# Performance work log

Measured on AMD Instinct MI355X. Metric: run time of the kernel, lower is better.

Reference implementation:

```python
import math
import jax, jax.numpy as jnp
from jax import lax
import numpy as np

NUM_EXPERTS = 8
TOP_K = 2
CAPACITY_FACTOR = 1.25
AUX_COEF = 0.01


def setup_inputs() -> dict:
    key = jax.random.key(0)
    k1, k2, k3, k4, k5 = jax.random.split(key, 5)
    B, T, C, I, E = 4, 2048, 768, 3072, NUM_EXPERTS
    x = jax.random.normal(k1, (B, T, C), dtype=jnp.float32)
    Wr = jax.random.normal(k2, (C, E), dtype=jnp.float32) * 0.02
    Wg = jax.random.normal(k3, (E, C, I), dtype=jnp.float32) * 0.02
    Wu = jax.random.normal(k4, (E, C, I), dtype=jnp.float32) * 0.02
    Wp = jax.random.normal(k5, (E, I, C), dtype=jnp.float32) * 0.02
    return {"x": x, "Wr": Wr, "Wg": Wg, "Wu": Wu, "Wp": Wp}


def reference(x, Wr, Wg, Wu, Wp):
    E, K = NUM_EXPERTS, TOP_K
    B, T, C = x.shape
    N = B * T
    capacity = max(1, math.ceil(CAPACITY_FACTOR * N / E))  # static: 1280
    xf = x.reshape(N, C)

    # --- router ---
    logits = xf @ Wr                                    # [N, E]
    probs = jax.nn.softmax(logits.astype(jnp.float32), axis=-1)
    gates, idx = lax.top_k(probs, K)                    # [N, 2] each
    gates = gates / jnp.clip(jnp.sum(gates, axis=-1, keepdims=True), 1e-9)

    # --- aux load-balancing loss ---
    oh1 = jax.nn.one_hot(idx[:, 0], E, dtype=jnp.int32)  # [N, E]
    oh2 = jax.nn.one_hot(idx[:, 1], E, dtype=jnp.int32)
    importance = probs.mean(axis=0)
    load = (oh1 + oh2).astype(jnp.float32).mean(axis=0) / K
    aux_loss = jnp.sum(importance * load) * E * AUX_COEF

    # --- capacity positions (running rank within each expert) ---
    pos1 = jnp.sum((jnp.cumsum(oh1, axis=0) - 1) * oh1, axis=-1)   # [N]
    mask1 = pos1 < capacity
    slot1 = idx[:, 0] * capacity + pos1
    count1 = jnp.minimum(jnp.sum(oh1, axis=0), capacity)           # [E]
    pos2 = jnp.sum((jnp.cumsum(oh2, axis=0) - 1) * oh2, axis=-1) + count1[idx[:, 1]]
    mask2 = pos2 < capacity
    slot2 = idx[:, 1] * capacity + pos2

    # --- dispatch (scatter into per-expert buffers; OOB slots dropped) ---
    buf = jnp.zeros((E * capacity, C), dtype=x.dtype)
    s1 = jnp.where(mask1, slot1, E * capacity)
    s2 = jnp.where(mask2, slot2, E * capacity)
    buf = buf.at[s1].set(xf, mode='drop')
    buf = buf.at[s2].set(xf, mode='drop')
    ein = buf.reshape(E, capacity, C)

    # --- per-expert swiglu MLP (grouped GEMMs) ---
    gate = jax.nn.silu(jnp.einsum('enc,ech->enh', ein, Wg))
    up = jnp.einsum('enc,ech->enh', ein, Wu)
    out = jnp.einsum('enh,ehc->enc', gate * up, Wp).reshape(E * capacity, C)

    # --- combine (gather back to token order, renormalized gates) ---
    g1 = gates[:, 0] * mask1.astype(jnp.float32)
    g2 = gates[:, 1] * mask2.astype(jnp.float32)
    denom = jnp.clip(g1 + g2, 1e-9)
    g1 = (g1 / denom).astype(x.dtype)
    g2 = (g2 / denom).astype(x.dtype)
    c1 = jnp.clip(slot1, 0, E * capacity - 1)
    c2 = jnp.clip(slot2, 0, E * capacity - 1)
    y = g1[:, None] * out[c1] + g2[:, None] * out[c2]
    return y.reshape(B, T, C), aux_loss
```

## Files before the change

kernel.cpp:

```cpp
#include <hip/hip_runtime.h>
#include <cstdint>
#include <cstddef>

#define NTOK 8192
#define NEXP 8
#define CAP 1280
#define CDIM 768
#define IDIM 3072
#define EROWS (NEXP*CAP)

typedef __attribute__((ext_vector_type(8))) short short8;
typedef __attribute__((ext_vector_type(4))) float f32x4;
typedef __attribute__((ext_vector_type(4))) unsigned short us4;
typedef __attribute__((ext_vector_type(8))) unsigned short us8;

__device__ __forceinline__ unsigned short f2b(float f) {
  unsigned u = __builtin_bit_cast(unsigned, f);
  u += 0x7FFFu + ((u >> 16) & 1u);
  return (unsigned short)(u >> 16);
}

__global__ __launch_bounds__(256) void transpose_cvt64(const float* __restrict__ src,
    unsigned short* __restrict__ dst, int R, int S) {
  int tilesS = S >> 6, tilesR = R >> 6;
  int perE = tilesR * tilesS;
  int e = blockIdx.x / perE;
  int rem = blockIdx.x % perE;
  int rt = rem / tilesS, st = rem % tilesS;
  const float* se = src + (size_t)e*R*S + ((size_t)rt*64)*S + st*64;
  unsigned short* de = dst + (size_t)e*R*S + ((size_t)st*64)*R + rt*64;
  __shared__ float tile[64][65];
  int c4 = (threadIdx.x & 15)*4, rr = threadIdx.x >> 4;
#pragma unroll
  for (int p = 0; p < 4; ++p) {
    float4 v = *(const float4*)(se + (size_t)(rr + 16*p)*S + c4);
    tile[rr + 16*p][c4+0] = v.x; tile[rr + 16*p][c4+1] = v.y;
    tile[rr + 16*p][c4+2] = v.z; tile[rr + 16*p][c4+3] = v.w;
  }
  __syncthreads();
#pragma unroll
  for (int p = 0; p < 4; ++p) {
    int s = rr + 16*p;
    us4 o;
    o.x = f2b(tile[c4+0][s]); o.y = f2b(tile[c4+1][s]);
    o.z = f2b(tile[c4+2][s]); o.w = f2b(tile[c4+3][s]);
    *(us4*)(de + (size_t)s*R + c4) = o;
  }
}

__global__ __launch_bounds__(256) void wgu_cvt64(const float* __restrict__ Wg,
    const float* __restrict__ Wu, unsigned short* __restrict__ Wgu) {
  const int tilesR = CDIM/64, tilesS = IDIM/64;
  const int perE = tilesR * tilesS;
  int sel = blockIdx.x / (NEXP*perE);
  int rem = blockIdx.x % (NEXP*perE);
  int e = rem / perE; int r2 = rem % perE;
  int rt = r2 / tilesS, st = r2 % tilesS;
  const float* se = (sel ? Wu : Wg) + (size_t)e*CDIM*IDIM + ((size_t)rt*64)*IDIM + st*64;
  __shared__ float tile[64][65];
  int c4 = (threadIdx.x & 15)*4, rr = threadIdx.x >> 4;
#pragma unroll
  for (int p = 0; p < 4; ++p) {
    float4 v = *(const float4*)(se + (size_t)(rr + 16*p)*IDIM + c4);
    tile[rr + 16*p][c4+0] = v.x; tile[rr + 16*p][c4+1] = v.y;
    tile[rr + 16*p][c4+2] = v.z; tile[rr + 16*p][c4+3] = v.w;
  }
  __syncthreads();
  unsigned short* dstE = Wgu + (size_t)e*(2*IDIM)*CDIM;
#pragma unroll
  for (int p = 0; p < 4; ++p) {
    int s = rr + 16*p;
    int np = 128*st + 32*(s>>4) + (s&15) + sel*16;
    us4 o;
    o.x = f2b(tile[c4+0][s]); o.y = f2b(tile[c4+1][s]);
    o.z = f2b(tile[c4+2][s]); o.w = f2b(tile[c4+3][s]);
    *(us4*)(dstE + (size_t)np*CDIM + rt*64 + c4) = o;
  }
}

__global__ __launch_bounds__(256) void router_kernel(const float* __restrict__ x,
    const float* __restrict__ Wr, float* __restrict__ probs,
    int* __restrict__ idx1, int* __restrict__ idx2,
    float* __restrict__ g1r, float* __restrict__ g2r) {
  __shared__ float WrT[NEXP*CDIM];
  for (int i = threadIdx.x; i < NEXP*CDIM; i += 256) {
    int c = i >> 3, e = i & 7;
    WrT[e*CDIM + c] = Wr[i];
  }
  __syncthreads();
  int w = threadIdx.x >> 6, l = threadIdx.x & 63;
  int t = blockIdx.x*4 + w;
  float acc[NEXP];
#pragma unroll
  for (int e = 0; e < NEXP; ++e) acc[e] = 0.f;
  for (int k = 0; k < CDIM/64; ++k) {
    float xv = x[(size_t)t*CDIM + k*64 + l];
#pragma unroll
    for (int e = 0; e < NEXP; ++e) acc[e] += xv * WrT[e*CDIM + k*64 + l];
  }
#pragma unroll
  for (int off = 32; off > 0; off >>= 1) {
#pragma unroll
    for (int e = 0; e < NEXP; ++e) acc[e] += __shfl_xor(acc[e], off);
  }
  if (l == 0) {
    float m = acc[0];
#pragma unroll
    for (int e = 1; e < NEXP; ++e) m = fmaxf(m, acc[e]);
    float p[NEXP]; float s = 0.f;
#pragma unroll
    for (int e = 0; e < NEXP; ++e) { p[e] = expf(acc[e] - m); s += p[e]; }
    float inv = 1.f / s;
#pragma unroll
    for (int e = 0; e < NEXP; ++e) { p[e] *= inv; probs[(size_t)t*NEXP + e] = p[e]; }
    int i1 = 0; float b1 = p[0];
#pragma unroll
    for (int e = 1; e < NEXP; ++e) if (p[e] > b1) { b1 = p[e]; i1 = e; }
    int i2 = -1; float b2 = -1e30f;
#pragma unroll
    for (int e = 0; e < NEXP; ++e) if (e != i1 && p[e] > b2) { b2 = p[e]; i2 = e; }
    float gs = fmaxf(b1 + b2, 1e-9f);
    g1r[t] = b1 / gs; g2r[t] = b2 / gs;
    idx1[t] = i1; idx2[t] = i2;
  }
}

__global__ __launch_bounds__(1024) void scan_kernel(
    const int* __restrict__ idx1, const int* __restrict__ idx2,
    const float* __restrict__ g1r, const float* __restrict__ g2r,
    const float* __restrict__ probs,
    int* __restrict__ bufmap,
    int* __restrict__ c1o, int* __restrict__ c2o,
    float* __restrict__ g1o, float* __restrict__ g2o,
    float* __restrict__ aux_out) {
  __shared__ unsigned int scanbuf[1024][9];
  __shared__ unsigned int totals[NEXP];
  int tid = threadIdx.x;
  int e1[8], e2[8];
  unsigned int cnt[NEXP];
#pragma unroll
  for (int k = 0; k < NEXP; ++k) cnt[k] = 0;
  for (int j = 0; j < 8; ++j) {
    int t = tid*8 + j;
    e1[j] = idx1[t]; e2[j] = idx2[t];
    cnt[e1[j]] += 1u;
    cnt[e2[j]] += (1u << 16);
  }
#pragma unroll
  for (int k = 0; k < NEXP; ++k) scanbuf[tid][k] = cnt[k];
  unsigned int run[NEXP];
#pragma unroll
  for (int k = 0; k < NEXP; ++k) run[k] = cnt[k];
  __syncthreads();
  for (int off = 1; off < 1024; off <<= 1) {
    unsigned int add[NEXP];
#pragma unroll
    for (int k = 0; k < NEXP; ++k) add[k] = 0;
    if (tid >= off) {
#pragma unroll
      for (int k = 0; k < NEXP; ++k) add[k] = scanbuf[tid - off][k];
    }
    __syncthreads();
#pragma unroll
    for (int k = 0; k < NEXP; ++k) { run[k] += add[k]; scanbuf[tid][k] = run[k]; }
    __syncthreads();
  }
  if (tid == 1023) {
#pragma unroll
    for (int k = 0; k < NEXP; ++k) totals[k] = run[k];
  }
  __syncthreads();
  unsigned int excl[NEXP];
#pragma unroll
  for (int k = 0; k < NEXP; ++k) excl[k] = run[k] - cnt[k];
  int cnt1c[NEXP];
#pragma unroll
  for (int k = 0; k < NEXP; ++k) cnt1c[k] = min((int)(totals[k] & 0xFFFFu), CAP);

  for (int j = 0; j < 8; ++j) {
    int t = tid*8 + j;
    int a = e1[j];
    int pos1 = (int)(excl[a] & 0xFFFFu); excl[a] += 1u;
    int slot1 = a*CAP + pos1;
    bool m1 = pos1 < CAP;
    if (m1) bufmap[slot1] = t;
    int b = e2[j];
    int pos2 = (int)(excl[b] >> 16) + cnt1c[b]; excl[b] += (1u << 16);
    int slot2 = b*CAP + pos2;
    bool m2 = pos2 < CAP;
    if (m2) bufmap[slot2] = t;
    float G1 = m1 ? g1r[t] : 0.f;
    float G2 = m2 ? g2r[t] : 0.f;
    float den = fmaxf(G1 + G2, 1e-9f);
    g1o[t] = G1 / den; g2o[t] = G2 / den;
    c1o[t] = min(slot1, EROWS - 1);
    c2o[t] = min(slot2, EROWS - 1);
  }

  float imp[NEXP];
#pragma unroll
  for (int k = 0; k < NEXP; ++k) imp[k] = 0.f;
  for (int j = 0; j < 8; ++j) {
    int t = tid*8 + j;
    const float4* pr = (const float4*)(probs + (size_t)t*NEXP);
    float4 a0 = pr[0], a1 = pr[1];
    imp[0] += a0.x; imp[1] += a0.y; imp[2] += a0.z; imp[3] += a0.w;
    imp[4] += a1.x; imp[5] += a1.y; imp[6] += a1.z; imp[7] += a1.w;
  }
  __syncthreads();
  float* fbuf = (float*)&scanbuf[0][0];
#pragma unroll
  for (int k = 0; k < NEXP; ++k) fbuf[tid*9 + k] = imp[k];
  __syncthreads();
  for (int s = 512; s >= 1; s >>= 1) {
    if (tid < s) {
#pragma unroll
      for (int k = 0; k < NEXP; ++k) fbuf[tid*9 + k] += fbuf[(tid + s)*9 + k];
    }
    __syncthreads();
  }
  if (tid == 0) {
    float aux = 0.f;
#pragma unroll
    for (int k = 0; k < NEXP; ++k) {
      float importance = fbuf[k] / (float)NTOK;
      float loadk = (float)((totals[k] & 0xFFFFu) + (totals[k] >> 16)) / ((float)NTOK * 2.0f);
      aux += importance * loadk;
    }
    aux_out[0] = aux * (float)NEXP * 0.01f;
  }
}

__global__ __launch_bounds__(192) void dispatch_kernel(const float* __restrict__ x,
    const int* __restrict__ bufmap, unsigned short* __restrict__ ein) {
  int r = blockIdx.x;
  int t = bufmap[r];
  int q = threadIdx.x;
  float4 v = make_float4(0.f, 0.f, 0.f, 0.f);
  if (t >= 0) v = ((const float4*)x)[(size_t)t*(CDIM/4) + q];
  us4 o;
  o.x = f2b(v.x); o.y = f2b(v.y); o.z = f2b(v.z); o.w = f2b(v.w);
  ((us4*)ein)[(size_t)r*(CDIM/4) + q] = o;
}

#define BAR  asm volatile("s_barrier" ::: "memory")
#define VMW(N) asm volatile("s_waitcnt vmcnt(" #N ")" ::: "memory")
#define P1 __builtin_amdgcn_s_setprio(1)
#define P0 __builtin_amdgcn_s_setprio(0)

template<int KD>
__global__ __launch_bounds__(512, 2) void gemm1_8ph(
    const unsigned short* __restrict__ A,
    const unsigned short* __restrict__ Bw,
    unsigned short* __restrict__ H) {
  constexpr int NT = KD/64;
  constexpr int NITER = NT/2;
  __shared__ unsigned short lds[65536];

  const int bid = blockIdx.x;
  const int chunk = gridDim.x >> 3;
  const int tile = (bid & 7)*chunk + (bid >> 3);
  const int e = tile / 120;
  const int rem = tile % 120;
  const int nt = rem / 5, mt = rem % 5;

  const int tid = threadIdx.x;
  const int l = tid & 63, wid = tid >> 6;
  const int wr = wid >> 2, wc = wid & 3;
  const int lrow = l & 15, khi = l >> 4;

  const unsigned short* Ab = A  + (size_t)e*CAP*KD    + (size_t)mt*256*KD;
  const unsigned short* Bb = Bw + (size_t)e*(2*IDIM)*KD + (size_t)nt*256*KD;

  const int srow = tid >> 3;
  const int scol = (tid & 7) ^ (srow & 7);
  const size_t lane_off = (size_t)srow*KD + scol*8;
  const int lds_st = wid*512;

#define STG(buf, op, half, kt) do { \
    const unsigned short* s_ = ((op) ? Bb : Ab) + lane_off + (size_t)(half)*128*KD + (size_t)(kt)*64; \
    unsigned short* d_ = (unsigned short*)lds + (buf)*32768 + (op)*16384 + (half)*8192 + lds_st; \
    __builtin_amdgcn_global_load_lds((const __attribute__((address_space(1))) void*)s_, \
        (__attribute__((address_space(3))) void*)d_, 16, 0, 0); \
    __builtin_amdgcn_global_load_lds((const __attribute__((address_space(1))) void*)(s_ + (size_t)64*KD), \
        (__attribute__((address_space(3))) void*)(d_ + 4096), 16, 0, 0); \
  } while(0)

  const int swz0 = ((khi    ) ^ (lrow & 7)) * 8;
  const int swz1 = ((4 + khi) ^ (lrow & 7)) * 8;
  const int abase = wr*8192 + lrow*64;
  const int bbase = 16384 + (wc>>1)*8192 + ((wc&1)*64 + lrow)*64;

#define LDA(buf, dst, mb) do { _Pragma("unroll") for (int m_=0;m_<4;++m_) { \
    dst[m_][0] = *(const short8*)(lds + (buf)*32768 + abase + ((mb)+m_)*1024 + swz0); \
    dst[m_][1] = *(const short8*)(lds + (buf)*32768 + abase + ((mb)+m_)*1024 + swz1); } } while(0)
#define LDB(buf, dst, nb) do { _Pragma("unroll") for (int n_=0;n_<2;++n_) { \
    dst[n_][0] = *(const short8*)(lds + (buf)*32768 + bbase + ((nb)+n_)*1024 + swz0); \
    dst[n_][1] = *(const short8*)(lds + (buf)*32768 + bbase + ((nb)+n_)*1024 + swz1); } } while(0)
#define QUAD(af, bf, mb, nb) do { _Pragma("unroll") for (int r_=0;r_<2;++r_) \
    _Pragma("unroll") for (int n_=0;n_<2;++n_) \
    _Pragma("unroll") for (int m_=0;m_<4;++m_) \
      acc[(mb)+m_][(nb)+n_] = __builtin_amdgcn_mfma_f32_16x16x32_bf16(af[m_][r_], bf[n_][r_], acc[(mb)+m_][(nb)+n_], 0,0,0); } while(0)

  f32x4 acc[8][4];
#pragma unroll
  for (int i = 0; i < 8; ++i)
#pragma unroll
    for (int j = 0; j < 4; ++j) acc[i][j] = (f32x4){0.f,0.f,0.f,0.f};

  short8 a[4][2], bl[2][2], bh[2][2];

  STG(0,0,0,0); STG(0,0,1,0); STG(0,1,0,0); STG(0,1,1,0);
  STG(1,1,0,1); STG(1,1,1,1); STG(1,0,0,1);
  VMW(6);
  BAR;

#define ITER(tY, t2, t3, DOS2, VM4, VM8) \
    LDA(0,a,0); LDB(0,bl,0); STG(1,0,1,(tY)); \
    BAR; P1; QUAD(a,bl,0,0); P0; BAR; \
    LDB(0,bh,2); \
    BAR; P1; QUAD(a,bh,0,2); P0; BAR; \
    LDA(0,a,4); if (DOS2) STG(0,1,0,(t2)); \
    BAR; P1; QUAD(a,bh,4,2); P0; BAR; \
    if (DOS2) STG(0,1,1,(t2)); VM4; \
    BAR; P1; QUAD(a,bl,4,0); P0; BAR; \
    LDA(1,a,0); LDB(1,bl,0); if (DOS2) STG(0,0,0,(t2)); \
    BAR; P1; QUAD(a,bl,0,0); P0; BAR; \
    LDB(1,bh,2); if (DOS2) STG(0,0,1,(t2)); \
    BAR; P1; QUAD(a,bh,0,2); P0; BAR; \
    LDA(1,a,4); if (DOS2) STG(1,1,0,(t3)); \
    BAR; P1; QUAD(a,bh,4,2); P0; BAR; \
    if (DOS2) { STG(1,1,1,(t3)); STG(1,0,0,(t3)); } VM8; \
    BAR; P1; QUAD(a,bl,4,0); P0; BAR;

#pragma unroll 1
  for (int i = 0; i < NITER-1; ++i) {
    const int tY = 2*i+1, t2 = 2*i+2, t3 = 2*i+3;
    ITER(tY, t2, t3, true, VMW(4), VMW(6));
  }
  ITER(NT-1, 0, 0, false, VMW(0), VMW(0));

#undef ITER
#undef QUAD
#undef LDB
#undef LDA
#undef STG

  __syncthreads();
  {
    const int cb0 = wc*32 + lrow;
    const int rb0 = wr*128 + khi*4;
#pragma unroll
    for (int m = 0; m < 8; ++m)
#pragma unroll
      for (int p = 0; p < 2; ++p) {
        f32x4 g = acc[m][2*p], u = acc[m][2*p+1];
#pragma unroll
        for (int r = 0; r < 4; ++r) {
          float gv = g[r];
          float hv = gv / (1.f + __expf(-gv)) * u[r];
          lds[(rb0 + m*16 + r)*136 + cb0 + p*16] = f2b(hv);
        }
      }
  }
  __syncthreads();
  const size_t rowg = (size_t)e*CAP + (size_t)mt*256;
  const size_t colg = (size_t)nt*128 + (size_t)(l & 15)*8;
#pragma unroll
  for (int i = 0; i < 8; ++i) {
    int row = wid*32 + i*4 + (l >> 4);
    us8 v = *(const us8*)(lds + row*136 + (l & 15)*8);
    *(us8*)(H + (rowg + row)*(size_t)IDIM + colg) = v;
  }
}

template<int K, bool NOUTER>
__global__ __launch_bounds__(256, 2) void gemm_bt(
    const unsigned short* __restrict__ A,
    const unsigned short* __restrict__ B0,
    float* __restrict__ Fout,
    int Ntiles, int N) {
  constexpr int MT = 10;
  int chunk = gridDim.x >> 3;
  int bid = blockIdx.x;
  int tile = (bid & 7)*chunk + (bid >> 3);
  int perE = MT * Ntiles;
  int e = tile / perE, rem = tile % perE;
  int mt, nt;
  if (NOUTER) { nt = rem / MT; mt = rem % MT; }
  else        { mt = rem / Ntiles; nt = rem % Ntiles; }

  const unsigned short* Ae  = A  + (size_t)e*CAP*K + (size_t)mt*128*K;
  const unsigned short* B0e = B0 + (size_t)e*N*K   + (size_t)nt*128*K;

  __shared__ unsigned short Alds[128*64];
  __shared__ unsigned short B0lds[128*64];

  int tid = threadIdx.x;
  int l = tid & 63, w = tid >> 6;
  int rbase = w*8 + (l >> 3);
  int csrc  = (l & 7) ^ ((l >> 3) & 7);
  size_t gbase = (size_t)rbase*K + (size_t)csrc*8;
  int ldsoff = w*512;

  f32x4 acc0[16];
#pragma unroll
  for (int i = 0; i < 16; ++i) acc0[i] = (f32x4){0.f,0.f,0.f,0.f};

  int wm = (w >> 1)*64, wn = (w & 1)*64;
  int lrow = l & 15, khi = l >> 4;

  for (int kt = 0; kt < K/64; ++kt) {
    const unsigned short* Ag  = Ae  + gbase + (size_t)kt*64;
    const unsigned short* Bg0 = B0e + gbase + (size_t)kt*64;
#pragma unroll
    for (int q = 0; q < 4; ++q) {
      __builtin_amdgcn_global_load_lds(
          (const __attribute__((address_space(1))) void*)(Ag + (size_t)q*32*K),
          (__attribute__((address_space(3))) void*)(Alds + ldsoff + q*2048), 16, 0, 0);
    }
#pragma unroll
    for (int q = 0; q < 4; ++q) {
      __builtin_amdgcn_global_load_lds(
          (const __attribute__((address_space(1))) void*)(Bg0 + (size_t)q*32*K),
          (__attribute__((address_space(3))) void*)(B0lds + ldsoff + q*2048), 16, 0, 0);
    }
    __syncthreads();
#pragma unroll
    for (int kk = 0; kk < 2; ++kk) {
      int cs = (kk*4 + khi) ^ (l & 7);
      short8 af[4];
#pragma unroll
      for (int m = 0; m < 4; ++m) {
        int row = wm + m*16 + lrow;
        af[m] = *(const short8*)(Alds + row*64 + cs*8);
      }
#pragma unroll
      for (int n = 0; n < 4; ++n) {
        int rowb = wn + n*16 + lrow;
        short8 b0 = *(const short8*)(B0lds + rowb*64 + cs*8);
#pragma unroll
        for (int m = 0; m < 4; ++m)
          acc0[m*4+n] = __builtin_amdgcn_mfma_f32_16x16x32_bf16(af[m], b0, acc0[m*4+n], 0, 0, 0);
      }
    }
    __syncthreads();
  }

  float* Fp = Fout + (size_t)e*CAP*N + (size_t)mt*128*N + (size_t)nt*128;
#pragma unroll
  for (int m = 0; m < 4; ++m) {
#pragma unroll
    for (int n = 0; n < 4; ++n) {
      f32x4 v = acc0[m*4+n];
#pragma unroll
      for (int r = 0; r < 4; ++r) {
        int row = wm + m*16 + khi*4 + r;
        int col = wn + n*16 + lrow;
        Fp[(size_t)row*N + col] = v[r];
      }
    }
  }
}

__global__ __launch_bounds__(192) void combine_kernel(const float* __restrict__ outbuf,
    const int* __restrict__ c1, const int* __restrict__ c2,
    const float* __restrict__ g1, const float* __restrict__ g2,
    float* __restrict__ y) {
  int t = blockIdx.x;
  int q = threadIdx.x;
  float f1 = g1[t], f2 = g2[t];
  int a = c1[t], b = c2[t];
  float4 va = ((const float4*)outbuf)[(size_t)a*(CDIM/4) + q];
  float4 vb = ((const float4*)outbuf)[(size_t)b*(CDIM/4) + q];
  float4 r;
  r.x = f1*va.x + f2*vb.x;
  r.y = f1*va.y + f2*vb.y;
  r.z = f1*va.z + f2*vb.z;
  r.w = f1*va.w + f2*vb.w;
  ((float4*)y)[(size_t)t*(CDIM/4) + q] = r;
}

extern "C" void kernel_launch(void* const* d_in, const int* in_sizes, int n_in,
                              void* d_out, int out_size, void* d_ws, size_t ws_size,
                              hipStream_t stream) {
  const float* x  = (const float*)d_in[0];
  const float* Wr = (const float*)d_in[1];
  const float* Wg = (const float*)d_in[2];
  const float* Wu = (const float*)d_in[3];
  const float* Wp = (const float*)d_in[4];
  float* y = (float*)d_out;

  char* p = (char*)d_ws;
  auto alloc = [&](size_t bytes) { char* r = p; p += (bytes + 255) & ~(size_t)255; return r; };
  unsigned short* WguT = (unsigned short*)alloc((size_t)NEXP*2*IDIM*CDIM*2);
  unsigned short* WpT  = (unsigned short*)alloc((size_t)NEXP*CDIM*IDIM*2);
  unsigned short* ein  = (unsigned short*)alloc((size_t)EROWS*CDIM*2);
  unsigned short* h    = (unsigned short*)alloc((size_t)EROWS*IDIM*2);
  float* outbuf = (float*)alloc((size_t)EROWS*CDIM*4);
  float* probs  = (float*)alloc((size_t)NTOK*NEXP*4);
  int* idx1 = (int*)alloc(NTOK*4);
  int* idx2 = (int*)alloc(NTOK*4);
  int* c1   = (int*)alloc(NTOK*4);
  int* c2   = (int*)alloc(NTOK*4);
  float* g1r = (float*)alloc(NTOK*4);
  float* g2r = (float*)alloc(NTOK*4);
  float* g1o = (float*)alloc(NTOK*4);
  float* g2o = (float*)alloc(NTOK*4);
  int* bufmap = (int*)alloc(EROWS*4);

  size_t required = (size_t)(p - (char*)d_ws);
  if (ws_size < required) return;

  hipMemsetAsync(bufmap, 0xFF, EROWS*sizeof(int), stream);

  wgu_cvt64<<<2*NEXP*(CDIM/64)*(IDIM/64), 256, 0, stream>>>(Wg, Wu, WguT);
  transpose_cvt64<<<NEXP*(IDIM/64)*(CDIM/64), 256, 0, stream>>>(Wp, WpT, IDIM, CDIM);

  router_kernel<<<NTOK/4, 256, 0, stream>>>(x, Wr, probs, idx1, idx2, g1r, g2r);
  scan_kernel<<<1, 1024, 0, stream>>>(idx1, idx2, g1r, g2r, probs, bufmap,
                                      c1, c2, g1o, g2o, y + (size_t)NTOK*CDIM);
  dispatch_kernel<<<EROWS, 192, 0, stream>>>(x, bufmap, ein);

  gemm1_8ph<CDIM><<<NEXP*5*(2*IDIM/256), 512, 0, stream>>>(ein, WguT, h);
  gemm_bt<IDIM, false><<<NEXP*10*(CDIM/128), 256, 0, stream>>>(
      h, WpT, outbuf, CDIM/128, CDIM);

  combine_kernel<<<NTOK, 192, 0, stream>>>(outbuf, c1, c2, g1o, g2o, y);
}
```

Measured before the change: 316.8 us.

## Triple-buffer B operand in gate/up GEMM and store down-proj output as bf16

The gate/up GEMM grows LDS from 128KB to 160KB so the weight operand gets three rotating buffers while A stays double-buffered. This lets weight tiles be prefetched further ahead and hides global load latency better. Separately, the down-projection GEMM now writes bf16 through an LDS-staged, coalesced store instead of scattered fp32 writes, and the combine kernel reads bf16. This halves output traffic but drops output precision to bf16 and may lower occupancy of the first GEMM.

```diff
diff --git a/kernel.cpp b/kernel.cpp
--- a/kernel.cpp
+++ b/kernel.cpp
@@ -18,6 +18,9 @@
   unsigned u = __builtin_bit_cast(unsigned, f);
   u += 0x7FFFu + ((u >> 16) & 1u);
   return (unsigned short)(u >> 16);
+}
+__device__ __forceinline__ float b2f(unsigned short u) {
+  return __builtin_bit_cast(float, ((unsigned)u) << 16);
 }
 
 __global__ __launch_bounds__(256) void transpose_cvt64(const float* __restrict__ src,
@@ -255,7 +258,7 @@
     unsigned short* __restrict__ H) {
   constexpr int NT = KD/64;
   constexpr int NITER = NT/2;
-  __shared__ unsigned short lds[65536];
+  __shared__ unsigned short lds[81920];
 
   const int bid = blockIdx.x;
   const int chunk = gridDim.x >> 3;
@@ -269,7 +272,7 @@
   const int wr = wid >> 2, wc = wid & 3;
   const int lrow = l & 15, khi = l >> 4;
 
-  const unsigned short* Ab = A  + (size_t)e*CAP*KD    + (size_t)mt*256*KD;
+  const unsigned short* Ab = A  + (size_t)e*CAP*KD      + (size_t)mt*256*KD;
   const unsigned short* Bb = Bw + (size_t)e*(2*IDIM)*KD + (size_t)nt*256*KD;
 
   const int srow = tid >> 3;
@@ -277,9 +280,9 @@
   const size_t lane_off = (size_t)srow*KD + scol*8;
   const int lds_st = wid*512;
 
-#define STG(buf, op, half, kt) do { \
-    const unsigned short* s_ = ((op) ? Bb : Ab) + lane_off + (size_t)(half)*128*KD + (size_t)(kt)*64; \
-    unsigned short* d_ = (unsigned short*)lds + (buf)*32768 + (op)*16384 + (half)*8192 + lds_st; \
+#define STG(dstu, srcp, half, kt) do { \
+    const unsigned short* s_ = (srcp) + lane_off + (size_t)(half)*128*KD + (size_t)(kt)*64; \
+    unsigned short* d_ = (unsigned short*)lds + (dstu) + (half)*8192 + lds_st; \
     __builtin_amdgcn_global_load_lds((const __attribute__((address_space(1))) void*)s_, \
         (__attribute__((address_space(3))) void*)d_, 16, 0, 0); \
     __builtin_amdgcn_global_load_lds((const __attribute__((address_space(1))) void*)(s_ + (size_t)64*KD), \
@@ -288,15 +291,15 @@
 
   const int swz0 = ((khi    ) ^ (lrow & 7)) * 8;
   const int swz1 = ((4 + khi) ^ (lrow & 7)) * 8;
-  const int abase = wr*8192 + lrow*64;
-  const int bbase = 16384 + (wc>>1)*8192 + ((wc&1)*64 + lrow)*64;
-
-#define LDA(buf, dst, mb) do { _Pragma("unroll") for (int m_=0;m_<4;++m_) { \
-    dst[m_][0] = *(const short8*)(lds + (buf)*32768 + abase + ((mb)+m_)*1024 + swz0); \
-    dst[m_][1] = *(const short8*)(lds + (buf)*32768 + abase + ((mb)+m_)*1024 + swz1); } } while(0)
-#define LDB(buf, dst, nb) do { _Pragma("unroll") for (int n_=0;n_<2;++n_) { \
-    dst[n_][0] = *(const short8*)(lds + (buf)*32768 + bbase + ((nb)+n_)*1024 + swz0); \
-    dst[n_][1] = *(const short8*)(lds + (buf)*32768 + bbase + ((nb)+n_)*1024 + swz1); } } while(0)
+  const int aoff = wr*8192 + lrow*64;
+  const int boff = (wc>>1)*8192 + ((wc&1)*64 + lrow)*64;
+
+#define LDA(ab, dst, mb) do { _Pragma("unroll") for (int m_=0;m_<4;++m_) { \
+    dst[m_][0] = *(const short8*)(lds + (ab) + aoff + ((mb)+m_)*1024 + swz0); \
+    dst[m_][1] = *(const short8*)(lds + (ab) + aoff + ((mb)+m_)*1024 + swz1); } } while(0)
+#define LDB(bb, dst, nb) do { _Pragma("unroll") for (int n_=0;n_<2;++n_) { \
+    dst[n_][0] = *(const short8*)(lds + (bb) + boff + ((nb)+n_)*1024 + swz0); \
+    dst[n_][1] = *(const short8*)(lds + (bb) + boff + ((nb)+n_)*1024 + swz1); } } while(0)
 #define QUAD(af, bf, mb, nb) do { _Pragma("unroll") for (int r_=0;r_<2;++r_) \
     _Pragma("unroll") for (int n_=0;n_<2;++n_) \
     _Pragma("unroll") for (int m_=0;m_<4;++m_) \
@@ -310,35 +313,40 @@
 
   short8 a[4][2], bl[2][2], bh[2][2];
 
-  STG(0,0,0,0); STG(0,0,1,0); STG(0,1,0,0); STG(0,1,1,0);
-  STG(1,1,0,1); STG(1,1,1,1); STG(1,0,0,1);
-  VMW(6);
+  int bA_ = 32768, bB_ = 49152, bC_ = 65536;
+
+  STG(0, Ab, 0, 0);      STG(bA_, Bb, 0, 0);
+  STG(0, Ab, 1, 0);      STG(bA_, Bb, 1, 0);
+  STG(16384, Ab, 0, 1);  STG(bB_, Bb, 0, 1);
+  STG(16384, Ab, 1, 1);  STG(bB_, Bb, 1, 1);
+  VMW(8);
   BAR;
 
-#define ITER(tY, t2, t3, DOS2, VM4, VM8) \
-    LDA(0,a,0); LDB(0,bl,0); STG(1,0,1,(tY)); \
-    BAR; P1; QUAD(a,bl,0,0); P0; BAR; \
-    LDB(0,bh,2); \
-    BAR; P1; QUAD(a,bh,0,2); P0; BAR; \
-    LDA(0,a,4); if (DOS2) STG(0,1,0,(t2)); \
-    BAR; P1; QUAD(a,bh,4,2); P0; BAR; \
-    if (DOS2) STG(0,1,1,(t2)); VM4; \
-    BAR; P1; QUAD(a,bl,4,0); P0; BAR; \
-    LDA(1,a,0); LDB(1,bl,0); if (DOS2) STG(0,0,0,(t2)); \
-    BAR; P1; QUAD(a,bl,0,0); P0; BAR; \
-    LDB(1,bh,2); if (DOS2) STG(0,0,1,(t2)); \
-    BAR; P1; QUAD(a,bh,0,2); P0; BAR; \
-    LDA(1,a,4); if (DOS2) STG(1,1,0,(t3)); \
-    BAR; P1; QUAD(a,bh,4,2); P0; BAR; \
-    if (DOS2) { STG(1,1,1,(t3)); STG(1,0,0,(t3)); } VM8; \
-    BAR; P1; QUAD(a,bl,4,0); P0; BAR;
+#define ITER(t2, t3, DOS, VM4, VM8) \
+    LDA(0, a, 0); LDB(bA_, bl, 0); if (DOS) STG(bC_, Bb, 0, (t2)); \
+    BAR; P1; QUAD(a, bl, 0, 0); P0; BAR; \
+    LDB(bA_, bh, 2); if (DOS) STG(bC_, Bb, 1, (t2)); \
+    BAR; P1; QUAD(a, bh, 0, 2); P0; BAR; \
+    LDA(0, a, 4); \
+    BAR; P1; QUAD(a, bh, 4, 2); P0; BAR; \
+    if (DOS) STG(0, Ab, 0, (t2)); VM4; \
+    BAR; P1; QUAD(a, bl, 4, 0); P0; BAR; \
+    LDA(16384, a, 0); LDB(bB_, bl, 0); if (DOS) { STG(0, Ab, 1, (t2)); STG(bA_, Bb, 0, (t3)); } \
+    BAR; P1; QUAD(a, bl, 0, 0); P0; BAR; \
+    LDB(bB_, bh, 2); if (DOS) STG(bA_, Bb, 1, (t3)); \
+    BAR; P1; QUAD(a, bh, 0, 2); P0; BAR; \
+    LDA(16384, a, 4); \
+    BAR; P1; QUAD(a, bh, 4, 2); P0; BAR; \
+    if (DOS) { STG(16384, Ab, 0, (t3)); STG(16384, Ab, 1, (t3)); } VM8; \
+    BAR; P1; QUAD(a, bl, 4, 0); P0; BAR;
 
 #pragma unroll 1
   for (int i = 0; i < NITER-1; ++i) {
-    const int tY = 2*i+1, t2 = 2*i+2, t3 = 2*i+3;
-    ITER(tY, t2, t3, true, VMW(4), VMW(6));
-  }
-  ITER(NT-1, 0, 0, false, VMW(0), VMW(0));
+    const int t2 = 2*i+2, t3 = 2*i+3;
+    ITER(t2, t3, true, VMW(6), VMW(8));
+    int tmp = bC_; bC_ = bB_; bB_ = bA_; bA_ = tmp;
+  }
+  ITER(0, 0, false, VMW(0), VMW(0));
 
 #undef ITER
 #undef QUAD
@@ -374,11 +382,11 @@
   }
 }
 
-template<int K, bool NOUTER>
+template<int K>
 __global__ __launch_bounds__(256, 2) void gemm_bt(
     const unsigned short* __restrict__ A,
     const unsigned short* __restrict__ B0,
-    float* __restrict__ Fout,
+    unsigned short* __restrict__ Fout,
     int Ntiles, int N) {
   constexpr int MT = 10;
   int chunk = gridDim.x >> 3;
@@ -386,15 +394,14 @@
   int tile = (bid & 7)*chunk + (bid >> 3);
   int perE = MT * Ntiles;
   int e = tile / perE, rem = tile % perE;
-  int mt, nt;
-  if (NOUTER) { nt = rem / MT; mt = rem % MT; }
-  else        { mt = rem / Ntiles; nt = rem % Ntiles; }
+  int mt = rem / Ntiles, nt = rem % Ntiles;
 
   const unsigned short* Ae  = A  + (size_t)e*CAP*K + (size_t)mt*128*K;
   const unsigned short* B0e = B0 + (size_t)e*N*K   + (size_t)nt*128*K;
 
-  __shared__ unsigned short Alds[128*64];
-  __shared__ unsigned short B0lds[128*64];
+  __shared__ unsigned short sh[16384];
+  unsigned short* Alds = sh;
+  unsigned short* B0lds = sh + 8192;
 
   int tid = threadIdx.x;
   int l = tid & 63, w = tid >> 6;
@@ -447,23 +454,34 @@
     __syncthreads();
   }
 
-  float* Fp = Fout + (size_t)e*CAP*N + (size_t)mt*128*N + (size_t)nt*128;
-#pragma unroll
-  for (int m = 0; m < 4; ++m) {
-#pragma unroll
-    for (int n = 0; n < 4; ++n) {
-      f32x4 v = acc0[m*4+n];
-#pragma unroll
-      for (int r = 0; r < 4; ++r) {
-        int row = wm + m*16 + khi*4 + r;
-        int col = wn + n*16 + lrow;
-        Fp[(size_t)row*N + col] = v[r];
-      }
-    }
-  }
-}
-
-__global__ __launch_bounds__(192) void combine_kernel(const float* __restrict__ outbuf,
+  const size_t rowg = (size_t)e*CAP + (size_t)mt*128;
+  const size_t colg = (size_t)nt*128;
+#pragma unroll
+  for (int h = 0; h < 2; ++h) {
+    if ((w >> 1) == h) {
+#pragma unroll
+      for (int m = 0; m < 4; ++m)
+#pragma unroll
+        for (int n = 0; n < 4; ++n) {
+          f32x4 v = acc0[m*4+n];
+#pragma unroll
+          for (int r = 0; r < 4; ++r)
+            sh[(m*16 + khi*4 + r)*136 + wn + n*16 + lrow] = f2b(v[r]);
+        }
+    }
+    __syncthreads();
+#pragma unroll
+    for (int jj = 0; jj < 4; ++jj) {
+      int idx = tid + 256*jj;
+      int rp = idx >> 4, ch = idx & 15;
+      us8 v = *(const us8*)(sh + rp*136 + ch*8);
+      *(us8*)(Fout + (rowg + h*64 + rp)*(size_t)N + colg + ch*8) = v;
+    }
+    __syncthreads();
+  }
+}
+
+__global__ __launch_bounds__(192) void combine_kernel(const unsigned short* __restrict__ outbuf,
     const int* __restrict__ c1, const int* __restrict__ c2,
     const float* __restrict__ g1, const float* __restrict__ g2,
     float* __restrict__ y) {
@@ -471,13 +489,13 @@
   int q = threadIdx.x;
   float f1 = g1[t], f2 = g2[t];
   int a = c1[t], b = c2[t];
-  float4 va = ((const float4*)outbuf)[(size_t)a*(CDIM/4) + q];
-  float4 vb = ((const float4*)outbuf)[(size_t)b*(CDIM/4) + q];
+  us4 va = ((const us4*)outbuf)[(size_t)a*(CDIM/4) + q];
+  us4 vb = ((const us4*)outbuf)[(size_t)b*(CDIM/4) + q];
   float4 r;
-  r.x = f1*va.x + f2*vb.x;
-  r.y = f1*va.y + f2*vb.y;
-  r.z = f1*va.z + f2*vb.z;
-  r.w = f1*va.w + f2*vb.w;
+  r.x = f1*b2f(va.x) + f2*b2f(vb.x);
+  r.y = f1*b2f(va.y) + f2*b2f(vb.y);
+  r.z = f1*b2f(va.z) + f2*b2f(vb.z);
+  r.w = f1*b2f(va.w) + f2*b2f(vb.w);
   ((float4*)y)[(size_t)t*(CDIM/4) + q] = r;
 }
 
@@ -497,7 +515,7 @@
   unsigned short* WpT  = (unsigned short*)alloc((size_t)NEXP*CDIM*IDIM*2);
   unsigned short* ein  = (unsigned short*)alloc((size_t)EROWS*CDIM*2);
   unsigned short* h    = (unsigned short*)alloc((size_t)EROWS*IDIM*2);
-  float* outbuf = (float*)alloc((size_t)EROWS*CDIM*4);
+  unsigned short* outbuf = (unsigned short*)alloc((size_t)EROWS*CDIM*2);
   float* probs  = (float*)alloc((size_t)NTOK*NEXP*4);
   int* idx1 = (int*)alloc(NTOK*4);
   int* idx2 = (int*)alloc(NTOK*4);
@@ -523,7 +541,7 @@
   dispatch_kernel<<<EROWS, 192, 0, stream>>>(x, bufmap, ein);
 
   gemm1_8ph<CDIM><<<NEXP*5*(2*IDIM/256), 512, 0, stream>>>(ein, WguT, h);
-  gemm_bt<IDIM, false><<<NEXP*10*(CDIM/128), 256, 0, stream>>>(
+  gemm_bt<IDIM><<<NEXP*10*(CDIM/128), 256, 0, stream>>>(
       h, WpT, outbuf, CDIM/128, CDIM);
 
   combine_kernel<<<NTOK, 192, 0, stream>>>(outbuf, c1, c2, g1o, g2o, y);
```

Result: no change. 312.8 us (-1.3%).
